# Kernel tuning notes

Measured on AMD Instinct MI355X. Metric: run time of the kernel, lower is better.

Reference implementation:

```python
import jax, jax.numpy as jnp
import numpy as np

N, E, IN, H0, H1 = 50000, 1600000, 64, 64, 128


def _gcn(h, W, b, row, col):
    # PyG GCNConv, add_self_loops=False, unit edge weights:
    # out[col] += d^{-1/2}[row] * d^{-1/2}[col] * (h @ W)[row]; bias added after aggregation
    n = h.shape[0]
    deg = jnp.zeros((n,), h.dtype).at[col].add(jnp.ones((row.shape[0],), h.dtype))
    dinv = jnp.where(deg > 0, jax.lax.rsqrt(jnp.maximum(deg, 1e-12)), 0.0)
    norm = (dinv[row] * dinv[col])[:, None]  # [E,1]
    m = h @ W  # transform before propagate (small GEMM)
    out = jnp.zeros((n, W.shape[1]), h.dtype).at[col].add(norm * m[row])
    return out + b


def _bn(h, g, b):
    # BatchNorm1d training-mode math (biased variance), eps=1e-5
    mu = h.mean(0)
    var = ((h - mu) ** 2).mean(0)
    return g * (h - mu) * jax.lax.rsqrt(var + 1e-5) + b


def _san(h):
    return jnp.nan_to_num(h, nan=0.0, posinf=100.0, neginf=-100.0)


def _slice(x, ei, W0, b0, W1, b1, res1, g0, be0, g1, be1):
    row, col = ei[0], ei[1]
    # layer 0: conv -> bn -> relu -> (dropout=eval identity) -> residual (Identity, 64==64) -> nan_to_num
    h1 = _san(jax.nn.relu(_bn(_gcn(x, W0, b0, row, col), g0, be0)) + x)
    # layer 1 (last): conv -> bn -> residual (Linear proj 64->128, no bias) -> nan_to_num
    h2 = _san(_bn(_gcn(h1, W1, b1, row, col), g1, be1) + h1 @ res1)
    return h2


def setup_inputs() -> dict:
    k = jax.random.split(jax.random.key(0), 16)
    f = lambda kk, sh, s: jax.random.normal(kk, sh, jnp.float32) * s
    return {
        "x": f(k[0], (N, IN), 1.0),
        "edge_index0": jax.random.randint(k[1], (2, E), 0, N),
        "edge_index1": jax.random.randint(k[2], (2, E), 0, N),
        "w0_s0": f(k[3], (IN, H0), 0.1), "b0_s0": jnp.zeros((H0,), jnp.float32),
        "w1_s0": f(k[4], (H0, H1), 0.1), "b1_s0": jnp.zeros((H1,), jnp.float32),
        "res1_s0": f(k[5], (H0, H1), 0.1),
        "w0_s1": f(k[6], (IN, H0), 0.1), "b0_s1": jnp.zeros((H0,), jnp.float32),
        "w1_s1": f(k[7], (H0, H1), 0.1), "b1_s1": jnp.zeros((H1,), jnp.float32),
        "res1_s1": f(k[8], (H0, H1), 0.1),
        "bn_g0": jnp.ones((H0,), jnp.float32), "bn_b0": jnp.zeros((H0,), jnp.float32),
        "bn_g1": jnp.ones((H1,), jnp.float32), "bn_b1": jnp.zeros((H1,), jnp.float32),
        "fc1_w": f(k[9], (2 * H1, H1), 0.1), "fc1_b": jnp.zeros((H1,), jnp.float32),
        "fc2_w": f(k[10], (H1, 2), 0.1), "fc2_b": jnp.zeros((2,), jnp.float32),
    }


def reference(x, edge_index0, edge_index1,
              w0_s0, b0_s0, w1_s0, b1_s0, res1_s0,
              w0_s1, b0_s1, w1_s1, b1_s1, res1_s1,
              bn_g0, bn_b0, bn_g1, bn_b1,
              fc1_w, fc1_b, fc2_w, fc2_b):
    out0 = _slice(x, edge_index0, w0_s0, b0_s0, w1_s0, b1_s0, res1_s0, bn_g0, bn_b0, bn_g1, bn_b1)
    out1 = _slice(x, edge_index1, w0_s1, b0_s1, w1_s1, b1_s1, res1_s1, bn_g0, bn_b0, bn_g1, bn_b1)
    combined = jnp.concatenate([out0, out1], axis=1)  # [N, 2*H1]
    h = jax.nn.relu(combined @ fc1_w + fc1_b)  # dropout is eval-mode identity
    logits = h @ fc2_w + fc2_b
    return logits, jax.nn.softmax(logits, axis=1)
```

## Files before the change

### kernel.cpp

```cpp
#include <hip/hip_runtime.h>
#include <hip/hip_bf16.h>
#include <math.h>


typedef short v8s __attribute__((ext_vector_type(8)));
typedef float f32x4 __attribute__((ext_vector_type(4)));

#define BSTRIDE 10240

__device__ __forceinline__ float sanf(float v) {
    if (v != v) return 0.f;
    if (isinf(v)) return v > 0.f ? 100.f : -100.f;
    return v;
}

__device__ __forceinline__ unsigned short bf16of(float v) {
    __hip_bfloat16 h = __float2bfloat16(v);
    return *(unsigned short*)&h;
}
__device__ __forceinline__ unsigned pack2(float lo, float hi) {
    return (unsigned)bf16of(lo) | ((unsigned)bf16of(hi) << 16);
}
__device__ __forceinline__ float uflo(unsigned u) { return __uint_as_float(u << 16); }
__device__ __forceinline__ float ufhi(unsigned u) { return __uint_as_float(u & 0xFFFF0000u); }
__device__ __forceinline__ float fofbf16(unsigned short u) {
    return __uint_as_float(((unsigned)u) << 16);
}

__device__ __forceinline__ void packone(const float* __restrict__ src, unsigned* __restrict__ dst,
                                        int L, int Khalf, int F) {
    int c = L / Khalf, kp = L - c * Khalf;
    dst[L] = pack2(src[(2 * kp) * F + c], src[(2 * kp + 1) * F + c]);
}

__global__ __launch_bounds__(256) void prep_kernel(const float* __restrict__ w0_0,
                                                   const float* __restrict__ w0_1,
                                                   const float* __restrict__ w1_0,
                                                   const float* __restrict__ w1_1,
                                                   const float* __restrict__ r_0,
                                                   const float* __restrict__ r_1,
                                                   const float* __restrict__ fc1,
                                                   unsigned* __restrict__ wpk,
                                                   int* __restrict__ bcnt,
                                                   float* __restrict__ sums) {
    int gid = blockIdx.x * 256 + threadIdx.x;
    if (gid < 512) bcnt[gid] = 0;
    if (gid < 8192) sums[gid] = 0.f;
    if (gid < 2048)       packone(w0_0, wpk + 0,     gid - 0,     32, 64);
    else if (gid < 4096)  packone(w0_1, wpk + 2048,  gid - 2048,  32, 64);
    else if (gid < 8192)  packone(w1_0, wpk + 4096,  gid - 4096,  32, 128);
    else if (gid < 12288) packone(w1_1, wpk + 8192,  gid - 8192,  32, 128);
    else if (gid < 16384) packone(r_0,  wpk + 12288, gid - 12288, 32, 128);
    else if (gid < 20480) packone(r_1,  wpk + 16384, gid - 16384, 32, 128);
    else if (gid < 36864) packone(fc1,  wpk + 20480, gid - 20480, 128, 128);
}


__global__ __launch_bounds__(512) void kC_bin(const int* __restrict__ ei0,
                                              const int* __restrict__ ei1,
                                              int* __restrict__ bcnt,
                                              unsigned* __restrict__ binned,
                                              int E, int n) {
    __shared__ int cnt[512];
    __shared__ int base[512];
    int t = threadIdx.x;
    cnt[t] = 0;
    int E2 = 2 * E;
    int e0 = blockIdx.x * 8192;
    unsigned pk[16];
    int bk[16];
    __syncthreads();
#pragma unroll
    for (int j = 0; j < 16; ++j) {
        int ge = e0 + t + j * 512;
        bk[j] = -1;
        if (ge < E2) {
            int slice = ge >= E;
            const int* ei = slice ? ei1 : ei0;
            int e = ge - slice * E;
            int col = ei[E + e], row = ei[e];
            int gcol = slice * n + col;
            bk[j] = gcol >> 8;
            pk[j] = (unsigned)row | (((unsigned)gcol & 255u) << 16);
            atomicAdd(&cnt[bk[j]], 1);
        }
    }
    __syncthreads();
    {
        int c = cnt[t];
        base[t] = c ? atomicAdd(&bcnt[t], c) : 0;
    }
    __syncthreads();
    cnt[t] = 0;
    __syncthreads();
#pragma unroll
    for (int j = 0; j < 16; ++j) {
        if (bk[j] >= 0) {
            int loc = atomicAdd(&cnt[bk[j]], 1);
            int off = base[bk[j]] + loc;
            if (off < BSTRIDE) binned[(size_t)bk[j] * BSTRIDE + off] = pk[j];
        }
    }
}

__global__ __launch_bounds__(512) void kD_build(const unsigned* __restrict__ binned,
                                                const int* __restrict__ bcnt,
                                                int* __restrict__ rowptr,
                                                float* __restrict__ dinv,
                                                unsigned short* __restrict__ csr,
                                                int n2, int NB) {
    __shared__ int pref[512];
    __shared__ int cnt[256];
    __shared__ int scn[256];
    __shared__ int cur[256];
    int b = blockIdx.x, t = threadIdx.x;
    pref[t] = (t < NB) ? bcnt[t] : 0;
    __syncthreads();
    for (int off = 1; off < 512; off <<= 1) {
        int u = (t >= off) ? pref[t - off] : 0;
        __syncthreads();
        pref[t] += u;
        __syncthreads();
    }
    int s = (b > 0) ? pref[b - 1] : 0;
    int e = pref[b];
    int m = e - s;
    const unsigned* seg = binned + (size_t)b * BSTRIDE;
    if (t < 256) cnt[t] = 0;
    __syncthreads();
    for (int i = t; i < m; i += 512) atomicAdd(&cnt[(seg[i] >> 16) & 255], 1);
    __syncthreads();
    int v = (t < 256) ? cnt[t] : 0;
    if (t < 256) scn[t] = v;
    __syncthreads();
    for (int off = 1; off < 256; off <<= 1) {
        int u = (t < 256 && t >= off) ? scn[t - off] : 0;
        __syncthreads();
        if (t < 256) scn[t] += u;
        __syncthreads();
    }
    if (t < 256) {
        int excl = scn[t] - v;
        int gcol = b * 256 + t;
        if (gcol < n2) {
            rowptr[gcol] = s + excl;
            dinv[gcol] = v > 0 ? rsqrtf((float)v) : 0.f;
        }
        cur[t] = excl;
    }
    __syncthreads();
    for (int i = t; i < m; i += 512) {
        unsigned p = seg[i];
        int cl = (p >> 16) & 255;
        int pos = s + atomicAdd(&cur[cl], 1);
        csr[pos] = (unsigned short)(p & 0xFFFFu);
    }
    if (b == 0 && t == 0) rowptr[n2] = pref[NB - 1];
}


__global__ __launch_bounds__(256) void prescale_bf(const float* __restrict__ x,
                                                   const float* __restrict__ dinv,
                                                   unsigned short* __restrict__ xsb,
                                                   int n64, int n) {
    int i8 = (blockIdx.x * 256 + threadIdx.x) * 8;
    if (i8 >= n64) return;
    int row = i8 >> 6;
    float4 v0 = *(const float4*)&x[i8];
    float4 v1 = *(const float4*)&x[i8 + 4];
    float d0 = dinv[row], d1 = dinv[n + row];
    uint4 o0, o1;
    o0.x = pack2(v0.x * d0, v0.y * d0); o0.y = pack2(v0.z * d0, v0.w * d0);
    o0.z = pack2(v1.x * d0, v1.y * d0); o0.w = pack2(v1.z * d0, v1.w * d0);
    o1.x = pack2(v0.x * d1, v0.y * d1); o1.y = pack2(v0.z * d1, v0.w * d1);
    o1.z = pack2(v1.x * d1, v1.y * d1); o1.w = pack2(v1.z * d1, v1.w * d1);
    *(uint4*)&xsb[i8] = o0;
    *(uint4*)&xsb[n64 + i8] = o1;
}

#define LOAD8(U, IDX)                                                       \
    do {                                                                    \
        _Pragma("unroll") for (int j = 0; j < 8; ++j) {                     \
            int r = __shfl((IDX), j, 8);                                    \
            (U)[j] = *(const uint4*)&mb[(size_t)r * 64 + l * 8];            \
        }                                                                   \
    } while (0)
#define ZPAD8(U, BB)                                                        \
    do {                                                                    \
        _Pragma("unroll") for (int j = 0; j < 8; ++j)                       \
            if ((BB) + j >= e) { (U)[j].x = 0; (U)[j].y = 0;                \
                                 (U)[j].z = 0; (U)[j].w = 0; }              \
    } while (0)
#define ACC8(U)                                                             \
    do {                                                                    \
        _Pragma("unroll") for (int j = 0; j < 8; ++j) {                     \
            a0 += uflo((U)[j].x); a1 += ufhi((U)[j].x);                     \
            a2 += uflo((U)[j].y); a3 += ufhi((U)[j].y);                     \
            a4 += uflo((U)[j].z); a5 += ufhi((U)[j].z);                     \
            a6 += uflo((U)[j].w); a7 += ufhi((U)[j].w);                     \
        }                                                                   \
    } while (0)

__global__ __launch_bounds__(256) void gatherbf_kernel(const int* __restrict__ rowptr,
                                                       const unsigned short* __restrict__ csr,
                                                       const unsigned short* __restrict__ xsb,
                                                       const float* __restrict__ dinv,
                                                       unsigned short* __restrict__ outb,
                                                       int n) {
    int blk = blockIdx.x;
    int xcd = blk & 7;
    int slice = (xcd >= 4) ? 1 : 0;
    int rank = (blk >> 3) * 4 + (xcd & 3);
    int nodeLocal = rank * 32 + (threadIdx.x >> 3);
    if (nodeLocal >= n) return;
    int node = slice * n + nodeLocal;
    int l = threadIdx.x & 7;
    const unsigned short* mb = xsb + (size_t)slice * n * 64;
    int s = rowptr[node], e = rowptr[node + 1];
    float a0 = 0.f, a1 = 0.f, a2 = 0.f, a3 = 0.f, a4 = 0.f, a5 = 0.f, a6 = 0.f, a7 = 0.f;
    uint4 uA[8], uB[8];
    int b = s;
    if (b + 8 <= e) {
        int ia = csr[b + l];
        LOAD8(uA, ia);
        int bB = b + 8;
        int ib = (bB + l < e) ? (int)csr[bB + l] : 0;
        while (true) {
            bool hasB = (bB < e);
            if (hasB) {
                LOAD8(uB, ib);
                if (bB + 8 > e) ZPAD8(uB, bB);
            }
            int bA2 = bB + 8;
            if (bA2 < e) ia = (bA2 + l < e) ? (int)csr[bA2 + l] : 0;
            ACC8(uA);
            if (!hasB) break;
            bool hasA2 = (bA2 < e);
            if (hasA2) {
                LOAD8(uA, ia);
                if (bA2 + 8 > e) ZPAD8(uA, bA2);
            }
            int bB2 = bA2 + 8;
            if (bB2 < e) ib = (bB2 + l < e) ? (int)csr[bB2 + l] : 0;
            ACC8(uB);
            if (!hasA2) break;
            bB = bB2;
        }
    } else if (b < e) {
        int ia = (b + l < e) ? (int)csr[b + l] : 0;
        LOAD8(uA, ia);
        ZPAD8(uA, b);
        ACC8(uA);
    }
    float d = dinv[node];
    uint4 o;
    o.x = pack2(a0 * d, a1 * d);
    o.y = pack2(a2 * d, a3 * d);
    o.z = pack2(a4 * d, a5 * d);
    o.w = pack2(a6 * d, a7 * d);
    *(uint4*)&outb[(size_t)node * 64 + l * 8] = o;
}


template <int F>
__global__ __launch_bounds__(256) void mfma_gemmb(const unsigned short* __restrict__ Ab,
                                                  const unsigned* __restrict__ WT0,
                                                  const unsigned* __restrict__ WT1,
                                                  unsigned short* __restrict__ Cb,
                                                  float* __restrict__ sums_base,
                                                  int roff, int n) {
    constexpr int NC = F / 16;
    __shared__ float ls[2 * F];
    __shared__ unsigned short stb[64 * F];
    int BPS = (n + 63) >> 6;
    int slice = blockIdx.x >= BPS;
    int sb = blockIdx.x - slice * BPS;
    const unsigned* WT = slice ? WT1 : WT0;
    int row0 = slice * n + sb * 64;
    int rows = min(64, n - sb * 64);
    for (int i = threadIdx.x; i < 2 * F; i += 256) ls[i] = 0.f;
    int w = threadIdx.x >> 6, lane = threadIdx.x & 63, q = lane >> 4, ln = lane & 15;
    const unsigned* A32 = (const unsigned*)Ab;
    size_t arow = (size_t)(row0 + 16 * w + ln) * 32;
    v8s af0 = *(const v8s*)&A32[arow + q * 4];
    v8s af1 = *(const v8s*)&A32[arow + 16 + q * 4];
    f32x4 acc[NC];
#pragma unroll
    for (int ct = 0; ct < NC; ++ct) acc[ct] = {0.f, 0.f, 0.f, 0.f};
#pragma unroll
    for (int ct = 0; ct < NC; ++ct) {
        v8s b0 = *(const v8s*)&WT[(ct * 16 + ln) * 32 + q * 4];
        v8s b1 = *(const v8s*)&WT[(ct * 16 + ln) * 32 + 16 + q * 4];
        acc[ct] = __builtin_amdgcn_mfma_f32_16x16x32_bf16(af0, b0, acc[ct], 0, 0, 0);
        acc[ct] = __builtin_amdgcn_mfma_f32_16x16x32_bf16(af1, b1, acc[ct], 0, 0, 0);
    }
    __syncthreads();
#pragma unroll
    for (int ct = 0; ct < NC; ++ct) {
        float s1 = 0.f, s2 = 0.f;
        int cc = ct * 16 + ln;
#pragma unroll
        for (int i = 0; i < 4; ++i) {
            int r = 16 * w + q * 4 + i;
            stb[r * F + (cc ^ ((r & 7) << 3))] = bf16of(acc[ct][i]);
            if (r < rows) {
                float v = acc[ct][i];
                s1 += v;
                s2 += v * v;
            }
        }
        s1 += __shfl_xor(s1, 16); s1 += __shfl_xor(s1, 32);
        s2 += __shfl_xor(s2, 16); s2 += __shfl_xor(s2, 32);
        if (q == 0) {
            atomicAdd(&ls[cc], s1);
            atomicAdd(&ls[F + cc], s2);
        }
    }
    __syncthreads();
    {
        constexpr int CPT = F / 4;
        int rr = threadIdx.x >> 2, sg = threadIdx.x & 3;
        if (rr < rows) {
            int swz = (rr & 7) << 3;
            int cb = sg * CPT;
            uint4* dst = (uint4*)(Cb + (size_t)(row0 + rr) * F + cb);
#pragma unroll
            for (int jj = 0; jj < CPT / 8; ++jj)
                dst[jj] = *(const uint4*)&stb[rr * F + ((cb + jj * 8) ^ swz)];
        }
    }
    if (threadIdx.x < F) {
        float* dst = sums_base + (blockIdx.x & 7) * 1024 + roff + slice * 2 * F;
        unsafeAtomicAdd(&dst[threadIdx.x], ls[threadIdx.x]);
        unsafeAtomicAdd(&dst[F + threadIdx.x], ls[F + threadIdx.x]);
    }
}

__global__ __launch_bounds__(256) void mfma_apply1(const unsigned short* __restrict__ h1b,
                                                   const unsigned short* __restrict__ Tb,
                                                   const unsigned* __restrict__ RT0,
                                                   const unsigned* __restrict__ RT1,
                                                   const float* __restrict__ sums_base,
                                                   const float* __restrict__ g,
                                                   const float* __restrict__ be,
                                                   unsigned short* __restrict__ comb, int n) {
    __shared__ float st[64 * 128];
    __shared__ float scl[256];
    int BPS = (n + 63) >> 6;
    int slice = blockIdx.x >= BPS;
    int sb = blockIdx.x - slice * BPS;
    const unsigned* WT = slice ? RT1 : RT0;
    int row0 = slice * n + sb * 64;
    int rows = min(64, n - sb * 64);
    int t = threadIdx.x;
    if (t < 128) {
        float s1 = 0.f, s2 = 0.f;
#pragma unroll
        for (int r = 0; r < 8; ++r) {
            const float* src = sums_base + r * 1024 + slice * 256;
            s1 += src[t];
            s2 += src[128 + t];
        }
        float inv_n = 1.0f / (float)n;
        float mu = s1 * inv_n;
        float var = fmaxf(s2 * inv_n - mu * mu, 0.f);
        float scale = g[t] * rsqrtf(var + 1e-5f);
        scl[t] = scale;
        scl[128 + t] = be[t] - mu * scale;
    }
    int w = t >> 6, lane = t & 63, q = lane >> 4, ln = lane & 15;
    const unsigned* A32 = (const unsigned*)h1b;
    size_t arow = (size_t)(row0 + 16 * w + ln) * 32;
    v8s af0 = *(const v8s*)&A32[arow + q * 4];
    v8s af1 = *(const v8s*)&A32[arow + 16 + q * 4];
    f32x4 acc[8];
#pragma unroll
    for (int ct = 0; ct < 8; ++ct) acc[ct] = {0.f, 0.f, 0.f, 0.f};
#pragma unroll
    for (int ct = 0; ct < 8; ++ct) {
        v8s b0 = *(const v8s*)&WT[(ct * 16 + ln) * 32 + q * 4];
        v8s b1 = *(const v8s*)&WT[(ct * 16 + ln) * 32 + 16 + q * 4];
        acc[ct] = __builtin_amdgcn_mfma_f32_16x16x32_bf16(af0, b0, acc[ct], 0, 0, 0);
        acc[ct] = __builtin_amdgcn_mfma_f32_16x16x32_bf16(af1, b1, acc[ct], 0, 0, 0);
    }
#pragma unroll
    for (int ct = 0; ct < 8; ++ct) {
        int cc = ct * 16 + ln;
#pragma unroll
        for (int i = 0; i < 4; ++i) {
            int r = 16 * w + q * 4 + i;
            st[r * 128 + (cc ^ ((r & 7) << 2))] = acc[ct][i];
        }
    }
    __syncthreads();
    int rr = t >> 2, sg = t & 3;
    if (rr >= rows) return;
    int swz = (rr & 7) << 2;
    int rg = row0 + rr;
    const uint4* tbp = (const uint4*)(Tb + (size_t)rg * 128 + sg * 32);
    const float* scb = scl + sg * 32;
    uint4* outp = (uint4*)(comb + (size_t)(rg - slice * n) * 256 + slice * 128 + sg * 32);
#pragma unroll
    for (int jj = 0; jj < 4; ++jj) {
        uint4 tv = tbp[jj];
        int base = sg * 32 + jj * 8;
        float4 a0 = *(const float4*)&st[rr * 128 + (base ^ swz)];
        float4 a1 = *(const float4*)&st[rr * 128 + ((base + 4) ^ swz)];
        float4 s0 = *(const float4*)&scb[jj * 8];
        float4 s1 = *(const float4*)&scb[jj * 8 + 4];
        float4 h0 = *(const float4*)&scb[128 + jj * 8];
        float4 h1v = *(const float4*)&scb[128 + jj * 8 + 4];
        float o0 = sanf(fmaf(uflo(tv.x), s0.x, h0.x) + a0.x);
        float o1 = sanf(fmaf(ufhi(tv.x), s0.y, h0.y) + a0.y);
        float o2 = sanf(fmaf(uflo(tv.y), s0.z, h0.z) + a0.z);
        float o3 = sanf(fmaf(ufhi(tv.y), s0.w, h0.w) + a0.w);
        float o4 = sanf(fmaf(uflo(tv.z), s1.x, h1v.x) + a1.x);
        float o5 = sanf(fmaf(ufhi(tv.z), s1.y, h1v.y) + a1.y);
        float o6 = sanf(fmaf(uflo(tv.w), s1.z, h1v.z) + a1.z);
        float o7 = sanf(fmaf(ufhi(tv.w), s1.w, h1v.w) + a1.w);
        uint4 ov;
        ov.x = pack2(o0, o1);
        ov.y = pack2(o2, o3);
        ov.z = pack2(o4, o5);
        ov.w = pack2(o6, o7);
        outp[jj] = ov;
    }
}

__global__ __launch_bounds__(256) void mfma_head_fc2(const unsigned short* __restrict__ comb,
                                                     const unsigned* __restrict__ FT,
                                                     const float* __restrict__ bias,
                                                     const float* __restrict__ w2,
                                                     const float* __restrict__ b2,
                                                     float* __restrict__ out, int n) {
    int row0 = blockIdx.x * 64;
    int rows = min(64, n - row0);
    int w = threadIdx.x >> 6, lane = threadIdx.x & 63, q = lane >> 4, ln = lane & 15;
    const unsigned* A32 = (const unsigned*)comb;
    size_t arow = (size_t)(row0 + 16 * w + ln) * 128;
    f32x4 acc[8];
#pragma unroll
    for (int ct = 0; ct < 8; ++ct) acc[ct] = {0.f, 0.f, 0.f, 0.f};
#pragma unroll
    for (int kt = 0; kt < 4; ++kt) {
        v8s af0 = *(const v8s*)&A32[arow + kt * 32 + q * 4];
        v8s af1 = *(const v8s*)&A32[arow + kt * 32 + 16 + q * 4];
#pragma unroll
        for (int ct = 0; ct < 8; ++ct) {
            v8s b0 = *(const v8s*)&FT[(ct * 16 + ln) * 128 + kt * 32 + q * 4];
            v8s b1 = *(const v8s*)&FT[(ct * 16 + ln) * 128 + kt * 32 + 16 + q * 4];
            acc[ct] = __builtin_amdgcn_mfma_f32_16x16x32_bf16(af0, b0, acc[ct], 0, 0, 0);
            acc[ct] = __builtin_amdgcn_mfma_f32_16x16x32_bf16(af1, b1, acc[ct], 0, 0, 0);
        }
    }
    float p0[4] = {0.f, 0.f, 0.f, 0.f}, p1[4] = {0.f, 0.f, 0.f, 0.f};
#pragma unroll
    for (int ct = 0; ct < 8; ++ct) {
        int c = ct * 16 + ln;
        float bi = bias[c];
        float w20 = w2[c * 2], w21 = w2[c * 2 + 1];
#pragma unroll
        for (int i = 0; i < 4; ++i) {
            float h = fmaxf(acc[ct][i] + bi, 0.f);
            p0[i] = fmaf(h, w20, p0[i]);
            p1[i] = fmaf(h, w21, p1[i]);
        }
    }
#pragma unroll
    for (int i = 0; i < 4; ++i) {
#pragma unroll
        for (int msk = 1; msk < 16; msk <<= 1) {
            p0[i] += __shfl_xor(p0[i], msk);
            p1[i] += __shfl_xor(p1[i], msk);
        }
    }
    if (ln == 0) {
        float bb0 = b2[0], bb1 = b2[1];
#pragma unroll
        for (int i = 0; i < 4; ++i) {
            int r = 16 * w + q * 4 + i;
            if (r >= rows) continue;
            int R = row0 + r;
            float l0 = p0[i] + bb0, l1 = p1[i] + bb1;
            float mx = fmaxf(l0, l1);
            float e0 = expf(l0 - mx), e1 = expf(l1 - mx);
            float inv = 1.0f / (e0 + e1);
            out[(size_t)R * 2] = l0;
            out[(size_t)R * 2 + 1] = l1;
            out[(size_t)2 * n + R * 2] = e0 * inv;
            out[(size_t)2 * n + R * 2 + 1] = e1 * inv;
        }
    }
}

__global__ __launch_bounds__(256) void apply0_kernel(const unsigned short* __restrict__ t0b,
                                                     const float* __restrict__ x,
                                                     const float* __restrict__ sums_base,
                                                     const float* __restrict__ g,
                                                     const float* __restrict__ be,
                                                     const float* __restrict__ dinv,
                                                     unsigned short* __restrict__ h1b,
                                                     unsigned short* __restrict__ h1sb,
                                                     int n64, int total, int n) {
    __shared__ float sc[256];
    int t = threadIdx.x;
    if (t < 128) {
        int slice = t >> 6, f = t & 63;
        float s1 = 0.f, s2 = 0.f;
#pragma unroll
        for (int r = 0; r < 8; ++r) {
            const float* src = sums_base + r * 1024 + 512 + slice * 128;
            s1 += src[f];
            s2 += src[64 + f];
        }
        float inv_n = 1.0f / (float)n;
        float mu = s1 * inv_n;
        float var = fmaxf(s2 * inv_n - mu * mu, 0.f);
        float scale = g[f] * rsqrtf(var + 1e-5f);
        sc[slice * 128 + f] = scale;
        sc[slice * 128 + 64 + f] = be[f] - mu * scale;
    }
    __syncthreads();
    int i8 = (blockIdx.x * 256 + t) * 8;
    if (i8 >= total) return;
    int slice = i8 >= n64;
    int f0 = i8 & 63;
    const float* scp = sc + slice * 128;
    uint4 tv = *(const uint4*)&t0b[i8];
    const float* xp = x + (i8 - slice * n64);
    float4 x0 = *(const float4*)xp;
    float4 x1 = *(const float4*)(xp + 4);
    float4 s0 = *(const float4*)&scp[f0];
    float4 s1 = *(const float4*)&scp[f0 + 4];
    float4 g0 = *(const float4*)&scp[64 + f0];
    float4 g1 = *(const float4*)&scp[64 + f0 + 4];
    float d = dinv[i8 >> 6];
    float tvv[8] = {uflo(tv.x), ufhi(tv.x), uflo(tv.y), ufhi(tv.y),
                    uflo(tv.z), ufhi(tv.z), uflo(tv.w), ufhi(tv.w)};
    float sa[8] = {s0.x, s0.y, s0.z, s0.w, s1.x, s1.y, s1.z, s1.w};
    float sh[8] = {g0.x, g0.y, g0.z, g0.w, g1.x, g1.y, g1.z, g1.w};
    float xv[8] = {x0.x, x0.y, x0.z, x0.w, x1.x, x1.y, x1.z, x1.w};
    unsigned po[4], ps[4];
#pragma unroll
    for (int j = 0; j < 4; ++j) {
        float a = sanf(fmaxf(fmaf(tvv[2 * j], sa[2 * j], sh[2 * j]), 0.f) + xv[2 * j]);
        float b = sanf(fmaxf(fmaf(tvv[2 * j + 1], sa[2 * j + 1], sh[2 * j + 1]), 0.f) + xv[2 * j + 1]);
        po[j] = pack2(a, b);
        ps[j] = pack2(a * d, b * d);
    }
    *(uint4*)&h1b[i8] = *(uint4*)po;
    *(uint4*)&h1sb[i8] = *(uint4*)ps;
}

static inline int cdiv(int a, int b) { return (a + b - 1) / b; }

extern "C" void kernel_launch(void* const* d_in, const int* in_sizes, int n_in,
                              void* d_out, int out_size, void* d_ws, size_t ws_size,
                              hipStream_t stream) {
    const float* x       = (const float*)d_in[0];
    const int*   ei0     = (const int*)d_in[1];
    const int*   ei1     = (const int*)d_in[2];
    const float* w0_s0   = (const float*)d_in[3];
    const float* w1_s0   = (const float*)d_in[5];
    const float* res1_s0 = (const float*)d_in[7];
    const float* w0_s1   = (const float*)d_in[8];
    const float* w1_s1   = (const float*)d_in[10];
    const float* res1_s1 = (const float*)d_in[12];
    const float* bn_g0   = (const float*)d_in[13];
    const float* bn_b0   = (const float*)d_in[14];
    const float* bn_g1   = (const float*)d_in[15];
    const float* bn_b1   = (const float*)d_in[16];
    const float* fc1_w   = (const float*)d_in[17];
    const float* fc1_b   = (const float*)d_in[18];
    const float* fc2_w   = (const float*)d_in[19];
    const float* fc2_b   = (const float*)d_in[20];
    float* out = (float*)d_out;

    int n = in_sizes[0] / 64;
    int E = in_sizes[1] / 2;
    int n2 = 2 * n, E2 = 2 * E;
    int n64 = n * 64;
    int NB = cdiv(n2, 256);
    int BPS = cdiv(n, 64);
    int GB = 8 * cdiv(cdiv(n, 32), 4);

    float* X1 = (float*)d_ws;
    float* S  = X1 + (size_t)n2 * 64;
    unsigned short* Gb   = (unsigned short*)(S + (size_t)n2 * 64);
    unsigned short* h1b  = Gb + (size_t)n2 * 64;
    unsigned short* comb = h1b + (size_t)n2 * 64;
    unsigned short* xsb  = comb + (size_t)n * 256;
    float* dinv = (float*)(xsb + (size_t)n * 128);
    float* sums = dinv + n2;
    float* scsh = sums + 8192;
    unsigned* wpk = (unsigned*)(scsh + 512);
    unsigned short* csr = (unsigned short*)(wpk + 36864);
    int* rowptr = (int*)(csr + (size_t)E2);
    int* bcnt   = rowptr + (n2 + 1);
    unsigned short* t0b = (unsigned short*)X1;
    unsigned short* Tb  = (unsigned short*)X1;
    unsigned* binned = (unsigned*)comb;
    unsigned short* h1sb = (unsigned short*)S;
    unsigned* w0T0 = wpk + 0,    *w0T1 = wpk + 2048;
    unsigned* w1T0 = wpk + 4096, *w1T1 = wpk + 8192;
    unsigned* rT0  = wpk + 12288,*rT1  = wpk + 16384;
    unsigned* fT   = wpk + 20480;

    prep_kernel<<<144, 256, 0, stream>>>(w0_s0, w0_s1, w1_s0, w1_s1,
                                         res1_s0, res1_s1, fc1_w, wpk, bcnt, sums);
    kC_bin<<<cdiv(E2, 8192), 512, 0, stream>>>(ei0, ei1, bcnt, binned, E, n);
    kD_build<<<NB, 512, 0, stream>>>(binned, bcnt, rowptr, dinv, csr, n2, NB);

    prescale_bf<<<cdiv(n64, 2048), 256, 0, stream>>>(x, dinv, xsb, n64, n);
    gatherbf_kernel<<<GB, 256, 0, stream>>>(rowptr, csr, xsb, dinv, Gb, n);
    mfma_gemmb<64><<<2 * BPS, 256, 0, stream>>>(Gb, w0T0, w0T1, t0b, sums, 512, n);
    apply0_kernel<<<cdiv(2 * n64, 2048), 256, 0, stream>>>(t0b, x, sums, bn_g0, bn_b0,
                                                           dinv, h1b, h1sb, n64, 2 * n64, n);

    gatherbf_kernel<<<GB, 256, 0, stream>>>(rowptr, csr, h1sb, dinv, Gb, n);
    mfma_gemmb<128><<<2 * BPS, 256, 0, stream>>>(Gb, w1T0, w1T1, Tb, sums, 0, n);
    mfma_apply1<<<2 * BPS, 256, 0, stream>>>(h1b, Tb, rT0, rT1, sums, bn_g1, bn_b1, comb, n);

    mfma_head_fc2<<<BPS, 256, 0, stream>>>(comb, fT, fc1_b, fc2_w, fc2_b, out, n);
}
```

Before: 353.5 us.

## Fuse all stages into one persistent cooperative kernel with grid syncs

Replaces the chain of ten separate kernel launches (prep, binning, CSR build, prescale, two gathers, two GEMMs, the two apply steps and the head) with a single persistent cooperative kernel. The stages are separated by grid-wide barriers and run as grid-stride loops over tiles, with shared memory reused through a union. The aim is to remove launch overhead and inter-kernel gaps. In exchange, grid size is capped by occupancy, barriers become grid syncs, per-block work changes (for example the binning chunk size), and register pressure from the merged kernel may lower occupancy.

```diff
diff --git a/kernel.cpp b/kernel.cpp
--- a/kernel.cpp
+++ b/kernel.cpp
@@ -1,6 +1,9 @@
 #include <hip/hip_runtime.h>
 #include <hip/hip_bf16.h>
+#include <hip/hip_cooperative_groups.h>
 #include <math.h>
+
+namespace cg = cooperative_groups;
 
 
 typedef short v8s __attribute__((ext_vector_type(8)));
@@ -13,7 +16,6 @@
     if (isinf(v)) return v > 0.f ? 100.f : -100.f;
     return v;
 }
-
 __device__ __forceinline__ unsigned short bf16of(float v) {
     __hip_bfloat16 h = __float2bfloat16(v);
     return *(unsigned short*)&h;
@@ -23,159 +25,35 @@
 }
 __device__ __forceinline__ float uflo(unsigned u) { return __uint_as_float(u << 16); }
 __device__ __forceinline__ float ufhi(unsigned u) { return __uint_as_float(u & 0xFFFF0000u); }
-__device__ __forceinline__ float fofbf16(unsigned short u) {
-    return __uint_as_float(((unsigned)u) << 16);
-}
+
+struct Params {
+    const float* x;
+    const int *ei0, *ei1;
+    const float *w0_0, *w0_1, *w1_0, *w1_1, *r_0, *r_1, *fc1;
+    const float *bn_g0, *bn_b0, *bn_g1, *bn_b1;
+    const float *fc1_b, *fc2_w, *fc2_b;
+    float* out;
+    unsigned short* t0b;
+    unsigned short *Gb, *h1b, *comb, *xsb, *h1sb;
+    float *dinv, *sums;
+    unsigned* wpk;
+    unsigned short* csr;
+    int *rowptr, *bcnt;
+    unsigned* binned;
+    int n, E, NB, BPS;
+};
+
+union SMemU {
+    struct { int cnt[512]; int base[512]; } c;
+    struct { int red[256]; int cnt[256]; int scn[256]; int cur[256]; } d;
+    struct { unsigned short stb[64 * 128]; } g;
+    struct { float st[64 * 128]; } a1;
+};
 
 __device__ __forceinline__ void packone(const float* __restrict__ src, unsigned* __restrict__ dst,
                                         int L, int Khalf, int F) {
     int c = L / Khalf, kp = L - c * Khalf;
     dst[L] = pack2(src[(2 * kp) * F + c], src[(2 * kp + 1) * F + c]);
-}
-
-__global__ __launch_bounds__(256) void prep_kernel(const float* __restrict__ w0_0,
-                                                   const float* __restrict__ w0_1,
-                                                   const float* __restrict__ w1_0,
-                                                   const float* __restrict__ w1_1,
-                                                   const float* __restrict__ r_0,
-                                                   const float* __restrict__ r_1,
-                                                   const float* __restrict__ fc1,
-                                                   unsigned* __restrict__ wpk,
-                                                   int* __restrict__ bcnt,
-                                                   float* __restrict__ sums) {
-    int gid = blockIdx.x * 256 + threadIdx.x;
-    if (gid < 512) bcnt[gid] = 0;
-    if (gid < 8192) sums[gid] = 0.f;
-    if (gid < 2048)       packone(w0_0, wpk + 0,     gid - 0,     32, 64);
-    else if (gid < 4096)  packone(w0_1, wpk + 2048,  gid - 2048,  32, 64);
-    else if (gid < 8192)  packone(w1_0, wpk + 4096,  gid - 4096,  32, 128);
-    else if (gid < 12288) packone(w1_1, wpk + 8192,  gid - 8192,  32, 128);
-    else if (gid < 16384) packone(r_0,  wpk + 12288, gid - 12288, 32, 128);
-    else if (gid < 20480) packone(r_1,  wpk + 16384, gid - 16384, 32, 128);
-    else if (gid < 36864) packone(fc1,  wpk + 20480, gid - 20480, 128, 128);
-}
-
-
-__global__ __launch_bounds__(512) void kC_bin(const int* __restrict__ ei0,
-                                              const int* __restrict__ ei1,
-                                              int* __restrict__ bcnt,
-                                              unsigned* __restrict__ binned,
-                                              int E, int n) {
-    __shared__ int cnt[512];
-    __shared__ int base[512];
-    int t = threadIdx.x;
-    cnt[t] = 0;
-    int E2 = 2 * E;
-    int e0 = blockIdx.x * 8192;
-    unsigned pk[16];
-    int bk[16];
-    __syncthreads();
-#pragma unroll
-    for (int j = 0; j < 16; ++j) {
-        int ge = e0 + t + j * 512;
-        bk[j] = -1;
-        if (ge < E2) {
-            int slice = ge >= E;
-            const int* ei = slice ? ei1 : ei0;
-            int e = ge - slice * E;
-            int col = ei[E + e], row = ei[e];
-            int gcol = slice * n + col;
-            bk[j] = gcol >> 8;
-            pk[j] = (unsigned)row | (((unsigned)gcol & 255u) << 16);
-            atomicAdd(&cnt[bk[j]], 1);
-        }
-    }
-    __syncthreads();
-    {
-        int c = cnt[t];
-        base[t] = c ? atomicAdd(&bcnt[t], c) : 0;
-    }
-    __syncthreads();
-    cnt[t] = 0;
-    __syncthreads();
-#pragma unroll
-    for (int j = 0; j < 16; ++j) {
-        if (bk[j] >= 0) {
-            int loc = atomicAdd(&cnt[bk[j]], 1);
-            int off = base[bk[j]] + loc;
-            if (off < BSTRIDE) binned[(size_t)bk[j] * BSTRIDE + off] = pk[j];
-        }
-    }
-}
-
-__global__ __launch_bounds__(512) void kD_build(const unsigned* __restrict__ binned,
-                                                const int* __restrict__ bcnt,
-                                                int* __restrict__ rowptr,
-                                                float* __restrict__ dinv,
-                                                unsigned short* __restrict__ csr,
-                                                int n2, int NB) {
-    __shared__ int pref[512];
-    __shared__ int cnt[256];
-    __shared__ int scn[256];
-    __shared__ int cur[256];
-    int b = blockIdx.x, t = threadIdx.x;
-    pref[t] = (t < NB) ? bcnt[t] : 0;
-    __syncthreads();
-    for (int off = 1; off < 512; off <<= 1) {
-        int u = (t >= off) ? pref[t - off] : 0;
-        __syncthreads();
-        pref[t] += u;
-        __syncthreads();
-    }
-    int s = (b > 0) ? pref[b - 1] : 0;
-    int e = pref[b];
-    int m = e - s;
-    const unsigned* seg = binned + (size_t)b * BSTRIDE;
-    if (t < 256) cnt[t] = 0;
-    __syncthreads();
-    for (int i = t; i < m; i += 512) atomicAdd(&cnt[(seg[i] >> 16) & 255], 1);
-    __syncthreads();
-    int v = (t < 256) ? cnt[t] : 0;
-    if (t < 256) scn[t] = v;
-    __syncthreads();
-    for (int off = 1; off < 256; off <<= 1) {
-        int u = (t < 256 && t >= off) ? scn[t - off] : 0;
-        __syncthreads();
-        if (t < 256) scn[t] += u;
-        __syncthreads();
-    }
-    if (t < 256) {
-        int excl = scn[t] - v;
-        int gcol = b * 256 + t;
-        if (gcol < n2) {
-            rowptr[gcol] = s + excl;
-            dinv[gcol] = v > 0 ? rsqrtf((float)v) : 0.f;
-        }
-        cur[t] = excl;
-    }
-    __syncthreads();
-    for (int i = t; i < m; i += 512) {
-        unsigned p = seg[i];
-        int cl = (p >> 16) & 255;
-        int pos = s + atomicAdd(&cur[cl], 1);
-        csr[pos] = (unsigned short)(p & 0xFFFFu);
-    }
-    if (b == 0 && t == 0) rowptr[n2] = pref[NB - 1];
-}
-
-
-__global__ __launch_bounds__(256) void prescale_bf(const float* __restrict__ x,
-                                                   const float* __restrict__ dinv,
-                                                   unsigned short* __restrict__ xsb,
-                                                   int n64, int n) {
-    int i8 = (blockIdx.x * 256 + threadIdx.x) * 8;
-    if (i8 >= n64) return;
-    int row = i8 >> 6;
-    float4 v0 = *(const float4*)&x[i8];
-    float4 v1 = *(const float4*)&x[i8 + 4];
-    float d0 = dinv[row], d1 = dinv[n + row];
-    uint4 o0, o1;
-    o0.x = pack2(v0.x * d0, v0.y * d0); o0.y = pack2(v0.z * d0, v0.w * d0);
-    o0.z = pack2(v1.x * d0, v1.y * d0); o0.w = pack2(v1.z * d0, v1.w * d0);
-    o1.x = pack2(v0.x * d1, v0.y * d1); o1.y = pack2(v0.z * d1, v0.w * d1);
-    o1.z = pack2(v1.x * d1, v1.y * d1); o1.w = pack2(v1.z * d1, v1.w * d1);
-    *(uint4*)&xsb[i8] = o0;
-    *(uint4*)&xsb[n64 + i8] = o1;
 }
 
 #define LOAD8(U, IDX)                                                       \
@@ -201,21 +79,12 @@
         }                                                                   \
     } while (0)
 
-__global__ __launch_bounds__(256) void gatherbf_kernel(const int* __restrict__ rowptr,
-                                                       const unsigned short* __restrict__ csr,
-                                                       const unsigned short* __restrict__ xsb,
-                                                       const float* __restrict__ dinv,
-                                                       unsigned short* __restrict__ outb,
-                                                       int n) {
-    int blk = blockIdx.x;
-    int xcd = blk & 7;
-    int slice = (xcd >= 4) ? 1 : 0;
-    int rank = (blk >> 3) * 4 + (xcd & 3);
-    int nodeLocal = rank * 32 + (threadIdx.x >> 3);
-    if (nodeLocal >= n) return;
-    int node = slice * n + nodeLocal;
-    int l = threadIdx.x & 7;
-    const unsigned short* mb = xsb + (size_t)slice * n * 64;
+__device__ __forceinline__ void gather_node(const int* __restrict__ rowptr,
+                                            const unsigned short* __restrict__ csr,
+                                            const unsigned short* __restrict__ mb,
+                                            const float* __restrict__ dinv,
+                                            int node, int l,
+                                            unsigned short* __restrict__ outrow) {
     int s = rowptr[node], e = rowptr[node + 1];
     float a0 = 0.f, a1 = 0.f, a2 = 0.f, a3 = 0.f, a4 = 0.f, a5 = 0.f, a6 = 0.f, a7 = 0.f;
     uint4 uA[8], uB[8];
@@ -258,298 +127,444 @@
     o.y = pack2(a2 * d, a3 * d);
     o.z = pack2(a4 * d, a5 * d);
     o.w = pack2(a6 * d, a7 * d);
-    *(uint4*)&outb[(size_t)node * 64 + l * 8] = o;
-}
-
+    *(uint4*)&outrow[l * 8] = o;
+}
 
 template <int F>
-__global__ __launch_bounds__(256) void mfma_gemmb(const unsigned short* __restrict__ Ab,
-                                                  const unsigned* __restrict__ WT0,
-                                                  const unsigned* __restrict__ WT1,
-                                                  unsigned short* __restrict__ Cb,
-                                                  float* __restrict__ sums_base,
-                                                  int roff, int n) {
+__device__ __forceinline__ void gemm_tiles(const unsigned short* __restrict__ Ab,
+                                           const unsigned* __restrict__ WT0,
+                                           const unsigned* __restrict__ WT1,
+                                           unsigned short* __restrict__ Cb,
+                                           float* __restrict__ sums,
+                                           int roff, int n, int BPS,
+                                           unsigned short* stb, float* ls) {
     constexpr int NC = F / 16;
-    __shared__ float ls[2 * F];
-    __shared__ unsigned short stb[64 * F];
-    int BPS = (n + 63) >> 6;
-    int slice = blockIdx.x >= BPS;
-    int sb = blockIdx.x - slice * BPS;
-    const unsigned* WT = slice ? WT1 : WT0;
-    int row0 = slice * n + sb * 64;
-    int rows = min(64, n - sb * 64);
-    for (int i = threadIdx.x; i < 2 * F; i += 256) ls[i] = 0.f;
-    int w = threadIdx.x >> 6, lane = threadIdx.x & 63, q = lane >> 4, ln = lane & 15;
-    const unsigned* A32 = (const unsigned*)Ab;
-    size_t arow = (size_t)(row0 + 16 * w + ln) * 32;
-    v8s af0 = *(const v8s*)&A32[arow + q * 4];
-    v8s af1 = *(const v8s*)&A32[arow + 16 + q * 4];
-    f32x4 acc[NC];
-#pragma unroll
-    for (int ct = 0; ct < NC; ++ct) acc[ct] = {0.f, 0.f, 0.f, 0.f};
-#pragma unroll
-    for (int ct = 0; ct < NC; ++ct) {
-        v8s b0 = *(const v8s*)&WT[(ct * 16 + ln) * 32 + q * 4];
-        v8s b1 = *(const v8s*)&WT[(ct * 16 + ln) * 32 + 16 + q * 4];
-        acc[ct] = __builtin_amdgcn_mfma_f32_16x16x32_bf16(af0, b0, acc[ct], 0, 0, 0);
-        acc[ct] = __builtin_amdgcn_mfma_f32_16x16x32_bf16(af1, b1, acc[ct], 0, 0, 0);
-    }
-    __syncthreads();
-#pragma unroll
-    for (int ct = 0; ct < NC; ++ct) {
+    const int t = threadIdx.x;
+    const int G = gridDim.x;
+    for (int tile = blockIdx.x; tile < 2 * BPS; tile += G) {
+        int slice = tile >= BPS;
+        int sb = tile - slice * BPS;
+        const unsigned* WT = slice ? WT1 : WT0;
+        int row0 = slice * n + sb * 64;
+        int rows = min(64, n - sb * 64);
+        for (int i = t; i < 2 * F; i += 256) ls[i] = 0.f;
+        int w = t >> 6, lane = t & 63, q = lane >> 4, ln = lane & 15;
+        const unsigned* A32 = (const unsigned*)Ab;
+        size_t arow = (size_t)(row0 + 16 * w + ln) * 32;
+        v8s af0 = *(const v8s*)&A32[arow + q * 4];
+        v8s af1 = *(const v8s*)&A32[arow + 16 + q * 4];
+        f32x4 acc[NC];
+#pragma unroll
+        for (int ct = 0; ct < NC; ++ct) acc[ct] = {0.f, 0.f, 0.f, 0.f};
+#pragma unroll
+        for (int ct = 0; ct < NC; ++ct) {
+            v8s b0 = *(const v8s*)&WT[(ct * 16 + ln) * 32 + q * 4];
+            v8s b1 = *(const v8s*)&WT[(ct * 16 + ln) * 32 + 16 + q * 4];
+            acc[ct] = __builtin_amdgcn_mfma_f32_16x16x32_bf16(af0, b0, acc[ct], 0, 0, 0);
+            acc[ct] = __builtin_amdgcn_mfma_f32_16x16x32_bf16(af1, b1, acc[ct], 0, 0, 0);
+        }
+        __syncthreads();
+#pragma unroll
+        for (int ct = 0; ct < NC; ++ct) {
+            float s1 = 0.f, s2 = 0.f;
+            int cc = ct * 16 + ln;
+#pragma unroll
+            for (int i = 0; i < 4; ++i) {
+                int r = 16 * w + q * 4 + i;
+                stb[r * F + (cc ^ ((r & 7) << 3))] = bf16of(acc[ct][i]);
+                if (r < rows) {
+                    float v = acc[ct][i];
+                    s1 += v;
+                    s2 += v * v;
+                }
+            }
+            s1 += __shfl_xor(s1, 16); s1 += __shfl_xor(s1, 32);
+            s2 += __shfl_xor(s2, 16); s2 += __shfl_xor(s2, 32);
+            if (q == 0) {
+                atomicAdd(&ls[cc], s1);
+                atomicAdd(&ls[F + cc], s2);
+            }
+        }
+        __syncthreads();
+        {
+            constexpr int CPT = F / 4;
+            int rr = t >> 2, sg = t & 3;
+            if (rr < rows) {
+                int swz = (rr & 7) << 3;
+                int cb = sg * CPT;
+                uint4* dst = (uint4*)(Cb + (size_t)(row0 + rr) * F + cb);
+#pragma unroll
+                for (int jj = 0; jj < CPT / 8; ++jj)
+                    dst[jj] = *(const uint4*)&stb[rr * F + ((cb + jj * 8) ^ swz)];
+            }
+        }
+        if (t < F) {
+            float* dst = sums + (blockIdx.x & 7) * 1024 + roff + slice * 2 * F;
+            unsafeAtomicAdd(&dst[t], ls[t]);
+            unsafeAtomicAdd(&dst[F + t], ls[F + t]);
+        }
+        __syncthreads();
+    }
+}
+
+__global__ __launch_bounds__(256, 4) void fused_all(Params p) {
+    cg::grid_group grid = cg::this_grid();
+    __shared__ SMemU sm;
+    __shared__ float scl[512];
+    const int t = threadIdx.x;
+    const int bid = blockIdx.x;
+    const int G = gridDim.x;
+    const int n = p.n, E = p.E;
+    const int n2 = 2 * n, E2 = 2 * E, n64 = n * 64;
+    const int NB = p.NB, BPS = p.BPS;
+    unsigned* w0T0 = p.wpk + 0,    *w0T1 = p.wpk + 2048;
+    unsigned* w1T0 = p.wpk + 4096, *w1T1 = p.wpk + 8192;
+    unsigned* rT0  = p.wpk + 12288,*rT1  = p.wpk + 16384;
+    unsigned* fT   = p.wpk + 20480;
+
+    for (int gid = bid * 256 + t; gid < 36864; gid += G * 256) {
+        if (gid < 512) p.bcnt[gid] = 0;
+        if (gid < 8192) p.sums[gid] = 0.f;
+        if (gid < 2048)       packone(p.w0_0, p.wpk + 0,     gid - 0,     32, 64);
+        else if (gid < 4096)  packone(p.w0_1, p.wpk + 2048,  gid - 2048,  32, 64);
+        else if (gid < 8192)  packone(p.w1_0, p.wpk + 4096,  gid - 4096,  32, 128);
+        else if (gid < 12288) packone(p.w1_1, p.wpk + 8192,  gid - 8192,  32, 128);
+        else if (gid < 16384) packone(p.r_0,  p.wpk + 12288, gid - 12288, 32, 128);
+        else if (gid < 20480) packone(p.r_1,  p.wpk + 16384, gid - 16384, 32, 128);
+        else                  packone(p.fc1,  p.wpk + 20480, gid - 20480, 128, 128);
+    }
+    grid.sync();
+
+    {
+        int nch = (E2 + 4095) >> 12;
+        for (int ch = bid; ch < nch; ch += G) {
+            sm.c.cnt[t] = 0; sm.c.cnt[t + 256] = 0;
+            __syncthreads();
+            unsigned pk[16]; int bk[16];
+            int e0 = ch * 4096;
+#pragma unroll
+            for (int j = 0; j < 16; ++j) {
+                int ge = e0 + t + j * 256;
+                bk[j] = -1;
+                if (ge < E2) {
+                    int slice = ge >= E;
+                    const int* ei = slice ? p.ei1 : p.ei0;
+                    int e = ge - slice * E;
+                    int col = ei[E + e], row = ei[e];
+                    int gcol = slice * n + col;
+                    bk[j] = gcol >> 8;
+                    pk[j] = (unsigned)row | (((unsigned)gcol & 255u) << 16);
+                    atomicAdd(&sm.c.cnt[bk[j]], 1);
+                }
+            }
+            __syncthreads();
+            for (int i = t; i < 512; i += 256) {
+                int c = sm.c.cnt[i];
+                sm.c.base[i] = c ? atomicAdd(&p.bcnt[i], c) : 0;
+            }
+            __syncthreads();
+            sm.c.cnt[t] = 0; sm.c.cnt[t + 256] = 0;
+            __syncthreads();
+#pragma unroll
+            for (int j = 0; j < 16; ++j) {
+                if (bk[j] >= 0) {
+                    int loc = atomicAdd(&sm.c.cnt[bk[j]], 1);
+                    int off = sm.c.base[bk[j]] + loc;
+                    if (off < BSTRIDE) p.binned[(size_t)bk[j] * BSTRIDE + off] = pk[j];
+                }
+            }
+            __syncthreads();
+        }
+    }
+    grid.sync();
+
+    for (int b = bid; b < NB; b += G) {
+        int partial = 0;
+        for (int i = t; i < b; i += 256) partial += p.bcnt[i];
+        sm.d.red[t] = partial;
+        __syncthreads();
+        for (int off = 128; off > 0; off >>= 1) {
+            if (t < off) sm.d.red[t] += sm.d.red[t + off];
+            __syncthreads();
+        }
+        int s = sm.d.red[0];
+        int e = s + p.bcnt[b];
+        int m = e - s;
+        const unsigned* seg = p.binned + (size_t)b * BSTRIDE;
+        sm.d.cnt[t] = 0;
+        __syncthreads();
+        for (int i = t; i < m; i += 256) atomicAdd(&sm.d.cnt[(seg[i] >> 16) & 255], 1);
+        __syncthreads();
+        int v = sm.d.cnt[t];
+        sm.d.scn[t] = v;
+        __syncthreads();
+        for (int off = 1; off < 256; off <<= 1) {
+            int u = (t >= off) ? sm.d.scn[t - off] : 0;
+            __syncthreads();
+            sm.d.scn[t] += u;
+            __syncthreads();
+        }
+        {
+            int excl = sm.d.scn[t] - v;
+            int gcol = b * 256 + t;
+            if (gcol < n2) {
+                p.rowptr[gcol] = s + excl;
+                p.dinv[gcol] = v > 0 ? rsqrtf((float)v) : 0.f;
+            }
+            sm.d.cur[t] = excl;
+        }
+        __syncthreads();
+        for (int i = t; i < m; i += 256) {
+            unsigned pkv = seg[i];
+            int cl = (pkv >> 16) & 255;
+            int pos = s + atomicAdd(&sm.d.cur[cl], 1);
+            p.csr[pos] = (unsigned short)(pkv & 0xFFFFu);
+        }
+        if (b == NB - 1 && t == 0) p.rowptr[n2] = e;
+        __syncthreads();
+    }
+    grid.sync();
+
+    for (int i8 = (bid * 256 + t) * 8; i8 < n64; i8 += G * 256 * 8) {
+        int row = i8 >> 6;
+        float4 v0 = *(const float4*)&p.x[i8];
+        float4 v1 = *(const float4*)&p.x[i8 + 4];
+        float d0 = p.dinv[row], d1 = p.dinv[n + row];
+        uint4 o0, o1;
+        o0.x = pack2(v0.x * d0, v0.y * d0); o0.y = pack2(v0.z * d0, v0.w * d0);
+        o0.z = pack2(v1.x * d0, v1.y * d0); o0.w = pack2(v1.z * d0, v1.w * d0);
+        o1.x = pack2(v0.x * d1, v0.y * d1); o1.y = pack2(v0.z * d1, v0.w * d1);
+        o1.z = pack2(v1.x * d1, v1.y * d1); o1.w = pack2(v1.z * d1, v1.w * d1);
+        *(uint4*)&p.xsb[i8] = o0;
+        *(uint4*)&p.xsb[n64 + i8] = o1;
+    }
+    grid.sync();
+
+    {
+        int l = t & 7;
+        for (int base = bid * 32; base < n2; base += G * 32) {
+            int node = base + (t >> 3);
+            if (node < n2) {
+                const unsigned short* mb = p.xsb + (size_t)((node >= n) ? n : 0) * 64;
+                gather_node(p.rowptr, p.csr, mb, p.dinv, node, l, p.Gb + (size_t)node * 64);
+            }
+        }
+    }
+    grid.sync();
+
+    gemm_tiles<64>(p.Gb, w0T0, w0T1, p.t0b, p.sums, 512, n, BPS, sm.g.stb, scl);
+    grid.sync();
+
+    if (t < 128) {
+        int slice = t >> 6, f = t & 63;
         float s1 = 0.f, s2 = 0.f;
-        int cc = ct * 16 + ln;
-#pragma unroll
-        for (int i = 0; i < 4; ++i) {
-            int r = 16 * w + q * 4 + i;
-            stb[r * F + (cc ^ ((r & 7) << 3))] = bf16of(acc[ct][i]);
-            if (r < rows) {
-                float v = acc[ct][i];
-                s1 += v;
-                s2 += v * v;
-            }
-        }
-        s1 += __shfl_xor(s1, 16); s1 += __shfl_xor(s1, 32);
-        s2 += __shfl_xor(s2, 16); s2 += __shfl_xor(s2, 32);
-        if (q == 0) {
-            atomicAdd(&ls[cc], s1);
-            atomicAdd(&ls[F + cc], s2);
-        }
-    }
-    __syncthreads();
-    {
-        constexpr int CPT = F / 4;
-        int rr = threadIdx.x >> 2, sg = threadIdx.x & 3;
-        if (rr < rows) {
-            int swz = (rr & 7) << 3;
-            int cb = sg * CPT;
-            uint4* dst = (uint4*)(Cb + (size_t)(row0 + rr) * F + cb);
-#pragma unroll
-            for (int jj = 0; jj < CPT / 8; ++jj)
-                dst[jj] = *(const uint4*)&stb[rr * F + ((cb + jj * 8) ^ swz)];
-        }
-    }
-    if (threadIdx.x < F) {
-        float* dst = sums_base + (blockIdx.x & 7) * 1024 + roff + slice * 2 * F;
-        unsafeAtomicAdd(&dst[threadIdx.x], ls[threadIdx.x]);
-        unsafeAtomicAdd(&dst[F + threadIdx.x], ls[F + threadIdx.x]);
-    }
-}
-
-__global__ __launch_bounds__(256) void mfma_apply1(const unsigned short* __restrict__ h1b,
-                                                   const unsigned short* __restrict__ Tb,
-                                                   const unsigned* __restrict__ RT0,
-                                                   const unsigned* __restrict__ RT1,
-                                                   const float* __restrict__ sums_base,
-                                                   const float* __restrict__ g,
-                                                   const float* __restrict__ be,
-                                                   unsigned short* __restrict__ comb, int n) {
-    __shared__ float st[64 * 128];
-    __shared__ float scl[256];
-    int BPS = (n + 63) >> 6;
-    int slice = blockIdx.x >= BPS;
-    int sb = blockIdx.x - slice * BPS;
-    const unsigned* WT = slice ? RT1 : RT0;
-    int row0 = slice * n + sb * 64;
-    int rows = min(64, n - sb * 64);
-    int t = threadIdx.x;
-    if (t < 128) {
-        float s1 = 0.f, s2 = 0.f;
 #pragma unroll
         for (int r = 0; r < 8; ++r) {
-            const float* src = sums_base + r * 1024 + slice * 256;
-            s1 += src[t];
-            s2 += src[128 + t];
+            const float* src = p.sums + r * 1024 + 512 + slice * 128;
+            s1 += src[f];
+            s2 += src[64 + f];
         }
         float inv_n = 1.0f / (float)n;
         float mu = s1 * inv_n;
         float var = fmaxf(s2 * inv_n - mu * mu, 0.f);
-        float scale = g[t] * rsqrtf(var + 1e-5f);
-        scl[t] = scale;
-        scl[128 + t] = be[t] - mu * scale;
-    }
-    int w = t >> 6, lane = t & 63, q = lane >> 4, ln = lane & 15;
-    const unsigned* A32 = (const unsigned*)h1b;
-    size_t arow = (size_t)(row0 + 16 * w + ln) * 32;
-    v8s af0 = *(const v8s*)&A32[arow + q * 4];
-    v8s af1 = *(const v8s*)&A32[arow + 16 + q * 4];
-    f32x4 acc[8];
-#pragma unroll
-    for (int ct = 0; ct < 8; ++ct) acc[ct] = {0.f, 0.f, 0.f, 0.f};
-#pragma unroll
-    for (int ct = 0; ct < 8; ++ct) {
-        v8s b0 = *(const v8s*)&WT[(ct * 16 + ln) * 32 + q * 4];
-        v8s b1 = *(const v8s*)&WT[(ct * 16 + ln) * 32 + 16 + q * 4];
-        acc[ct] = __builtin_amdgcn_mfma_f32_16x16x32_bf16(af0, b0, acc[ct], 0, 0, 0);
-        acc[ct] = __builtin_amdgcn_mfma_f32_16x16x32_bf16(af1, b1, acc[ct], 0, 0, 0);
-    }
-#pragma unroll
-    for (int ct = 0; ct < 8; ++ct) {
-        int cc = ct * 16 + ln;
-#pragma unroll
-        for (int i = 0; i < 4; ++i) {
-            int r = 16 * w + q * 4 + i;
-            st[r * 128 + (cc ^ ((r & 7) << 2))] = acc[ct][i];
-        }
+        float scale = p.bn_g0[f] * rsqrtf(var + 1e-5f);
+        scl[slice * 128 + f] = scale;
+        scl[slice * 128 + 64 + f] = p.bn_b0[f] - mu * scale;
     }
     __syncthreads();
-    int rr = t >> 2, sg = t & 3;
-    if (rr >= rows) return;
-    int swz = (rr & 7) << 2;
-    int rg = row0 + rr;
-    const uint4* tbp = (const uint4*)(Tb + (size_t)rg * 128 + sg * 32);
-    const float* scb = scl + sg * 32;
-    uint4* outp = (uint4*)(comb + (size_t)(rg - slice * n) * 256 + slice * 128 + sg * 32);
-#pragma unroll
-    for (int jj = 0; jj < 4; ++jj) {
-        uint4 tv = tbp[jj];
-        int base = sg * 32 + jj * 8;
-        float4 a0 = *(const float4*)&st[rr * 128 + (base ^ swz)];
-        float4 a1 = *(const float4*)&st[rr * 128 + ((base + 4) ^ swz)];
-        float4 s0 = *(const float4*)&scb[jj * 8];
-        float4 s1 = *(const float4*)&scb[jj * 8 + 4];
-        float4 h0 = *(const float4*)&scb[128 + jj * 8];
-        float4 h1v = *(const float4*)&scb[128 + jj * 8 + 4];
-        float o0 = sanf(fmaf(uflo(tv.x), s0.x, h0.x) + a0.x);
-        float o1 = sanf(fmaf(ufhi(tv.x), s0.y, h0.y) + a0.y);
-        float o2 = sanf(fmaf(uflo(tv.y), s0.z, h0.z) + a0.z);
-        float o3 = sanf(fmaf(ufhi(tv.y), s0.w, h0.w) + a0.w);
-        float o4 = sanf(fmaf(uflo(tv.z), s1.x, h1v.x) + a1.x);
-        float o5 = sanf(fmaf(ufhi(tv.z), s1.y, h1v.y) + a1.y);
-        float o6 = sanf(fmaf(uflo(tv.w), s1.z, h1v.z) + a1.z);
-        float o7 = sanf(fmaf(ufhi(tv.w), s1.w, h1v.w) + a1.w);
-        uint4 ov;
-        ov.x = pack2(o0, o1);
-        ov.y = pack2(o2, o3);
-        ov.z = pack2(o4, o5);
-        ov.w = pack2(o6, o7);
-        outp[jj] = ov;
-    }
-}
-
-__global__ __launch_bounds__(256) void mfma_head_fc2(const unsigned short* __restrict__ comb,
-                                                     const unsigned* __restrict__ FT,
-                                                     const float* __restrict__ bias,
-                                                     const float* __restrict__ w2,
-                                                     const float* __restrict__ b2,
-                                                     float* __restrict__ out, int n) {
-    int row0 = blockIdx.x * 64;
-    int rows = min(64, n - row0);
-    int w = threadIdx.x >> 6, lane = threadIdx.x & 63, q = lane >> 4, ln = lane & 15;
-    const unsigned* A32 = (const unsigned*)comb;
-    size_t arow = (size_t)(row0 + 16 * w + ln) * 128;
-    f32x4 acc[8];
-#pragma unroll
-    for (int ct = 0; ct < 8; ++ct) acc[ct] = {0.f, 0.f, 0.f, 0.f};
-#pragma unroll
-    for (int kt = 0; kt < 4; ++kt) {
-        v8s af0 = *(const v8s*)&A32[arow + kt * 32 + q * 4];
-        v8s af1 = *(const v8s*)&A32[arow + kt * 32 + 16 + q * 4];
-#pragma unroll
-        for (int ct = 0; ct < 8; ++ct) {
-            v8s b0 = *(const v8s*)&FT[(ct * 16 + ln) * 128 + kt * 32 + q * 4];
-            v8s b1 = *(const v8s*)&FT[(ct * 16 + ln) * 128 + kt * 32 + 16 + q * 4];
-            acc[ct] = __builtin_amdgcn_mfma_f32_16x16x32_bf16(af0, b0, acc[ct], 0, 0, 0);
-            acc[ct] = __builtin_amdgcn_mfma_f32_16x16x32_bf16(af1, b1, acc[ct], 0, 0, 0);
-        }
-    }
-    float p0[4] = {0.f, 0.f, 0.f, 0.f}, p1[4] = {0.f, 0.f, 0.f, 0.f};
-#pragma unroll
-    for (int ct = 0; ct < 8; ++ct) {
-        int c = ct * 16 + ln;
-        float bi = bias[c];
-        float w20 = w2[c * 2], w21 = w2[c * 2 + 1];
-#pragma unroll
-        for (int i = 0; i < 4; ++i) {
-            float h = fmaxf(acc[ct][i] + bi, 0.f);
-            p0[i] = fmaf(h, w20, p0[i]);
-            p1[i] = fmaf(h, w21, p1[i]);
-        }
-    }
-#pragma unroll
-    for (int i = 0; i < 4; ++i) {
-#pragma unroll
-        for (int msk = 1; msk < 16; msk <<= 1) {
-            p0[i] += __shfl_xor(p0[i], msk);
-            p1[i] += __shfl_xor(p1[i], msk);
-        }
-    }
-    if (ln == 0) {
-        float bb0 = b2[0], bb1 = b2[1];
-#pragma unroll
-        for (int i = 0; i < 4; ++i) {
-            int r = 16 * w + q * 4 + i;
-            if (r >= rows) continue;
-            int R = row0 + r;
-            float l0 = p0[i] + bb0, l1 = p1[i] + bb1;
-            float mx = fmaxf(l0, l1);
-            float e0 = expf(l0 - mx), e1 = expf(l1 - mx);
-            float inv = 1.0f / (e0 + e1);
-            out[(size_t)R * 2] = l0;
-            out[(size_t)R * 2 + 1] = l1;
-            out[(size_t)2 * n + R * 2] = e0 * inv;
-            out[(size_t)2 * n + R * 2 + 1] = e1 * inv;
-        }
-    }
-}
-
-__global__ __launch_bounds__(256) void apply0_kernel(const unsigned short* __restrict__ t0b,
-                                                     const float* __restrict__ x,
-                                                     const float* __restrict__ sums_base,
-                                                     const float* __restrict__ g,
-                                                     const float* __restrict__ be,
-                                                     const float* __restrict__ dinv,
-                                                     unsigned short* __restrict__ h1b,
-                                                     unsigned short* __restrict__ h1sb,
-                                                     int n64, int total, int n) {
-    __shared__ float sc[256];
-    int t = threadIdx.x;
-    if (t < 128) {
-        int slice = t >> 6, f = t & 63;
+    for (int i8 = (bid * 256 + t) * 8; i8 < 2 * n64; i8 += G * 256 * 8) {
+        int slice = i8 >= n64;
+        int f0 = i8 & 63;
+        const float* scp = scl + slice * 128;
+        uint4 tv = *(const uint4*)&p.t0b[i8];
+        const float* xp = p.x + (i8 - slice * n64);
+        float4 x0 = *(const float4*)xp;
+        float4 x1 = *(const float4*)(xp + 4);
+        float4 s0 = *(const float4*)&scp[f0];
+        float4 s1 = *(const float4*)&scp[f0 + 4];
+        float4 g0 = *(const float4*)&scp[64 + f0];
+        float4 g1 = *(const float4*)&scp[64 + f0 + 4];
+        float d = p.dinv[i8 >> 6];
+        float tvv[8] = {uflo(tv.x), ufhi(tv.x), uflo(tv.y), ufhi(tv.y),
+                        uflo(tv.z), ufhi(tv.z), uflo(tv.w), ufhi(tv.w)};
+        float sa[8] = {s0.x, s0.y, s0.z, s0.w, s1.x, s1.y, s1.z, s1.w};
+        float sh[8] = {g0.x, g0.y, g0.z, g0.w, g1.x, g1.y, g1.z, g1.w};
+        float xv[8] = {x0.x, x0.y, x0.z, x0.w, x1.x, x1.y, x1.z, x1.w};
+        unsigned po[4], ps[4];
+#pragma unroll
+        for (int j = 0; j < 4; ++j) {
+            float a = sanf(fmaxf(fmaf(tvv[2 * j], sa[2 * j], sh[2 * j]), 0.f) + xv[2 * j]);
+            float b2 = sanf(fmaxf(fmaf(tvv[2 * j + 1], sa[2 * j + 1], sh[2 * j + 1]), 0.f) + xv[2 * j + 1]);
+            po[j] = pack2(a, b2);
+            ps[j] = pack2(a * d, b2 * d);
+        }
+        *(uint4*)&p.h1b[i8] = *(uint4*)po;
+        *(uint4*)&p.h1sb[i8] = *(uint4*)ps;
+    }
+    grid.sync();
+
+    {
+        int l = t & 7;
+        for (int base = bid * 32; base < n2; base += G * 32) {
+            int node = base + (t >> 3);
+            if (node < n2) {
+                const unsigned short* mb = p.h1sb + (size_t)((node >= n) ? n : 0) * 64;
+                gather_node(p.rowptr, p.csr, mb, p.dinv, node, l, p.Gb + (size_t)node * 64);
+            }
+        }
+    }
+    grid.sync();
+
+    gemm_tiles<128>(p.Gb, w1T0, w1T1, p.t0b , p.sums, 0, n, BPS, sm.g.stb, scl);
+    grid.sync();
+
+    {
+        int slice = t >> 7, f = t & 127;
         float s1 = 0.f, s2 = 0.f;
 #pragma unroll
         for (int r = 0; r < 8; ++r) {
-            const float* src = sums_base + r * 1024 + 512 + slice * 128;
+            const float* src = p.sums + r * 1024 + slice * 256;
             s1 += src[f];
-            s2 += src[64 + f];
+            s2 += src[128 + f];
         }
         float inv_n = 1.0f / (float)n;
         float mu = s1 * inv_n;
         float var = fmaxf(s2 * inv_n - mu * mu, 0.f);
+        const float* g = p.bn_g1;
+        const float* be = p.bn_b1;
         float scale = g[f] * rsqrtf(var + 1e-5f);
-        sc[slice * 128 + f] = scale;
-        sc[slice * 128 + 64 + f] = be[f] - mu * scale;
+        scl[slice * 256 + f] = scale;
+        scl[slice * 256 + 128 + f] = be[f] - mu * scale;
     }
     __syncthreads();
-    int i8 = (blockIdx.x * 256 + t) * 8;
-    if (i8 >= total) return;
-    int slice = i8 >= n64;
-    int f0 = i8 & 63;
-    const float* scp = sc + slice * 128;
-    uint4 tv = *(const uint4*)&t0b[i8];
-    const float* xp = x + (i8 - slice * n64);
-    float4 x0 = *(const float4*)xp;
-    float4 x1 = *(const float4*)(xp + 4);
-    float4 s0 = *(const float4*)&scp[f0];
-    float4 s1 = *(const float4*)&scp[f0 + 4];
-    float4 g0 = *(const float4*)&scp[64 + f0];
-    float4 g1 = *(const float4*)&scp[64 + f0 + 4];
-    float d = dinv[i8 >> 6];
-    float tvv[8] = {uflo(tv.x), ufhi(tv.x), uflo(tv.y), ufhi(tv.y),
-                    uflo(tv.z), ufhi(tv.z), uflo(tv.w), ufhi(tv.w)};
-    float sa[8] = {s0.x, s0.y, s0.z, s0.w, s1.x, s1.y, s1.z, s1.w};
-    float sh[8] = {g0.x, g0.y, g0.z, g0.w, g1.x, g1.y, g1.z, g1.w};
-    float xv[8] = {x0.x, x0.y, x0.z, x0.w, x1.x, x1.y, x1.z, x1.w};
-    unsigned po[4], ps[4];
-#pragma unroll
-    for (int j = 0; j < 4; ++j) {
-        float a = sanf(fmaxf(fmaf(tvv[2 * j], sa[2 * j], sh[2 * j]), 0.f) + xv[2 * j]);
-        float b = sanf(fmaxf(fmaf(tvv[2 * j + 1], sa[2 * j + 1], sh[2 * j + 1]), 0.f) + xv[2 * j + 1]);
-        po[j] = pack2(a, b);
-        ps[j] = pack2(a * d, b * d);
-    }
-    *(uint4*)&h1b[i8] = *(uint4*)po;
-    *(uint4*)&h1sb[i8] = *(uint4*)ps;
+    for (int tile = bid; tile < 2 * BPS; tile += G) {
+        int slice = tile >= BPS;
+        int sb = tile - slice * BPS;
+        const unsigned* WT = slice ? rT1 : rT0;
+        int row0 = slice * n + sb * 64;
+        int rows = min(64, n - sb * 64);
+        int w = t >> 6, lane = t & 63, q = lane >> 4, ln = lane & 15;
+        const unsigned* A32 = (const unsigned*)p.h1b;
+        size_t arow = (size_t)(row0 + 16 * w + ln) * 32;
+        v8s af0 = *(const v8s*)&A32[arow + q * 4];
+        v8s af1 = *(const v8s*)&A32[arow + 16 + q * 4];
+        f32x4 acc[8];
+#pragma unroll
+        for (int ct = 0; ct < 8; ++ct) acc[ct] = {0.f, 0.f, 0.f, 0.f};
+#pragma unroll
+        for (int ct = 0; ct < 8; ++ct) {
+            v8s b0 = *(const v8s*)&WT[(ct * 16 + ln) * 32 + q * 4];
+            v8s b1 = *(const v8s*)&WT[(ct * 16 + ln) * 32 + 16 + q * 4];
+            acc[ct] = __builtin_amdgcn_mfma_f32_16x16x32_bf16(af0, b0, acc[ct], 0, 0, 0);
+            acc[ct] = __builtin_amdgcn_mfma_f32_16x16x32_bf16(af1, b1, acc[ct], 0, 0, 0);
+        }
+#pragma unroll
+        for (int ct = 0; ct < 8; ++ct) {
+            int cc = ct * 16 + ln;
+#pragma unroll
+            for (int i = 0; i < 4; ++i) {
+                int r = 16 * w + q * 4 + i;
+                sm.a1.st[r * 128 + (cc ^ ((r & 7) << 2))] = acc[ct][i];
+            }
+        }
+        __syncthreads();
+        int rr = t >> 2, sg = t & 3;
+        if (rr < rows) {
+            int swz = (rr & 7) << 2;
+            int rg = row0 + rr;
+            const uint4* tbp = (const uint4*)(p.t0b + (size_t)rg * 128 + sg * 32);
+            const float* scb = scl + slice * 256 + sg * 32;
+            uint4* outp = (uint4*)(p.comb + (size_t)(rg - slice * n) * 256 + slice * 128 + sg * 32);
+#pragma unroll
+            for (int jj = 0; jj < 4; ++jj) {
+                uint4 tv = tbp[jj];
+                int base = sg * 32 + jj * 8;
+                float4 a0 = *(const float4*)&sm.a1.st[rr * 128 + (base ^ swz)];
+                float4 a1 = *(const float4*)&sm.a1.st[rr * 128 + ((base + 4) ^ swz)];
+                float4 s0 = *(const float4*)&scb[jj * 8];
+                float4 s1 = *(const float4*)&scb[jj * 8 + 4];
+                float4 h0 = *(const float4*)&scb[128 + jj * 8];
+                float4 h1v = *(const float4*)&scb[128 + jj * 8 + 4];
+                float o0 = sanf(fmaf(uflo(tv.x), s0.x, h0.x) + a0.x);
+                float o1 = sanf(fmaf(ufhi(tv.x), s0.y, h0.y) + a0.y);
+                float o2 = sanf(fmaf(uflo(tv.y), s0.z, h0.z) + a0.z);
+                float o3 = sanf(fmaf(ufhi(tv.y), s0.w, h0.w) + a0.w);
+                float o4 = sanf(fmaf(uflo(tv.z), s1.x, h1v.x) + a1.x);
+                float o5 = sanf(fmaf(ufhi(tv.z), s1.y, h1v.y) + a1.y);
+                float o6 = sanf(fmaf(uflo(tv.w), s1.z, h1v.z) + a1.z);
+                float o7 = sanf(fmaf(ufhi(tv.w), s1.w, h1v.w) + a1.w);
+                uint4 ov;
+                ov.x = pack2(o0, o1);
+                ov.y = pack2(o2, o3);
+                ov.z = pack2(o4, o5);
+                ov.w = pack2(o6, o7);
+                outp[jj] = ov;
+            }
+        }
+        __syncthreads();
+    }
+    grid.sync();
+
+    for (int tile = bid; tile < BPS; tile += G) {
+        int row0 = tile * 64;
+        int rows = min(64, n - row0);
+        int w = t >> 6, lane = t & 63, q = lane >> 4, ln = lane & 15;
+        const unsigned* A32 = (const unsigned*)p.comb;
+        size_t arow = (size_t)(row0 + 16 * w + ln) * 128;
+        f32x4 acc[8];
+#pragma unroll
+        for (int ct = 0; ct < 8; ++ct) acc[ct] = {0.f, 0.f, 0.f, 0.f};
+#pragma unroll
+        for (int kt = 0; kt < 4; ++kt) {
+            v8s af0 = *(const v8s*)&A32[arow + kt * 32 + q * 4];
+            v8s af1 = *(const v8s*)&A32[arow + kt * 32 + 16 + q * 4];
+#pragma unroll
+            for (int ct = 0; ct < 8; ++ct) {
+                v8s b0 = *(const v8s*)&fT[(ct * 16 + ln) * 128 + kt * 32 + q * 4];
+                v8s b1 = *(const v8s*)&fT[(ct * 16 + ln) * 128 + kt * 32 + 16 + q * 4];
+                acc[ct] = __builtin_amdgcn_mfma_f32_16x16x32_bf16(af0, b0, acc[ct], 0, 0, 0);
+                acc[ct] = __builtin_amdgcn_mfma_f32_16x16x32_bf16(af1, b1, acc[ct], 0, 0, 0);
+            }
+        }
+        float p0[4] = {0.f, 0.f, 0.f, 0.f}, p1[4] = {0.f, 0.f, 0.f, 0.f};
+#pragma unroll
+        for (int ct = 0; ct < 8; ++ct) {
+            int c = ct * 16 + ln;
+            float bi = p.fc1_b[c];
+            float w20 = p.fc2_w[c * 2], w21 = p.fc2_w[c * 2 + 1];
+#pragma unroll
+            for (int i = 0; i < 4; ++i) {
+                float h = fmaxf(acc[ct][i] + bi, 0.f);
+                p0[i] = fmaf(h, w20, p0[i]);
+                p1[i] = fmaf(h, w21, p1[i]);
+            }
+        }
+#pragma unroll
+        for (int i = 0; i < 4; ++i) {
+#pragma unroll
+            for (int msk = 1; msk < 16; msk <<= 1) {
+                p0[i] += __shfl_xor(p0[i], msk);
+                p1[i] += __shfl_xor(p1[i], msk);
+            }
+        }
+        if (ln == 0) {
+            float bb0 = p.fc2_b[0], bb1 = p.fc2_b[1];
+#pragma unroll
+            for (int i = 0; i < 4; ++i) {
+                int r = 16 * w + q * 4 + i;
+                if (r >= rows) continue;
+                int R = row0 + r;
+                float l0 = p0[i] + bb0, l1 = p1[i] + bb1;
+                float mx = fmaxf(l0, l1);
+                float e0 = expf(l0 - mx), e1 = expf(l1 - mx);
+                float inv = 1.0f / (e0 + e1);
+                p.out[(size_t)R * 2] = l0;
+                p.out[(size_t)R * 2 + 1] = l1;
+                p.out[(size_t)2 * n + R * 2] = e0 * inv;
+                p.out[(size_t)2 * n + R * 2 + 1] = e1 * inv;
+            }
+        }
+    }
 }
 
 static inline int cdiv(int a, int b) { return (a + b - 1) / b; }
@@ -557,32 +572,32 @@
 extern "C" void kernel_launch(void* const* d_in, const int* in_sizes, int n_in,
                               void* d_out, int out_size, void* d_ws, size_t ws_size,
                               hipStream_t stream) {
-    const float* x       = (const float*)d_in[0];
-    const int*   ei0     = (const int*)d_in[1];
-    const int*   ei1     = (const int*)d_in[2];
-    const float* w0_s0   = (const float*)d_in[3];
-    const float* w1_s0   = (const float*)d_in[5];
-    const float* res1_s0 = (const float*)d_in[7];
-    const float* w0_s1   = (const float*)d_in[8];
-    const float* w1_s1   = (const float*)d_in[10];
-    const float* res1_s1 = (const float*)d_in[12];
-    const float* bn_g0   = (const float*)d_in[13];
-    const float* bn_b0   = (const float*)d_in[14];
-    const float* bn_g1   = (const float*)d_in[15];
-    const float* bn_b1   = (const float*)d_in[16];
-    const float* fc1_w   = (const float*)d_in[17];
-    const float* fc1_b   = (const float*)d_in[18];
-    const float* fc2_w   = (const float*)d_in[19];
-    const float* fc2_b   = (const float*)d_in[20];
-    float* out = (float*)d_out;
+    Params hp;
+    hp.x     = (const float*)d_in[0];
+    hp.ei0   = (const int*)d_in[1];
+    hp.ei1   = (const int*)d_in[2];
+    hp.w0_0  = (const float*)d_in[3];
+    hp.w1_0  = (const float*)d_in[5];
+    hp.r_0   = (const float*)d_in[7];
+    hp.w0_1  = (const float*)d_in[8];
+    hp.w1_1  = (const float*)d_in[10];
+    hp.r_1   = (const float*)d_in[12];
+    hp.bn_g0 = (const float*)d_in[13];
+    hp.bn_b0 = (const float*)d_in[14];
+    hp.bn_g1 = (const float*)d_in[15];
+    hp.bn_b1 = (const float*)d_in[16];
+    hp.fc1   = (const float*)d_in[17];
+    hp.fc1_b = (const float*)d_in[18];
+    hp.fc2_w = (const float*)d_in[19];
+    hp.fc2_b = (const float*)d_in[20];
+    hp.out   = (float*)d_out;
 
     int n = in_sizes[0] / 64;
     int E = in_sizes[1] / 2;
     int n2 = 2 * n, E2 = 2 * E;
-    int n64 = n * 64;
-    int NB = cdiv(n2, 256);
-    int BPS = cdiv(n, 64);
-    int GB = 8 * cdiv(cdiv(n, 32), 4);
+    hp.n = n; hp.E = E;
+    hp.NB = cdiv(n2, 256);
+    hp.BPS = cdiv(n, 64);
 
     float* X1 = (float*)d_ws;
     float* S  = X1 + (size_t)n2 * 64;
@@ -597,29 +612,31 @@
     unsigned short* csr = (unsigned short*)(wpk + 36864);
     int* rowptr = (int*)(csr + (size_t)E2);
     int* bcnt   = rowptr + (n2 + 1);
-    unsigned short* t0b = (unsigned short*)X1;
-    unsigned short* Tb  = (unsigned short*)X1;
-    unsigned* binned = (unsigned*)comb;
-    unsigned short* h1sb = (unsigned short*)S;
-    unsigned* w0T0 = wpk + 0,    *w0T1 = wpk + 2048;
-    unsigned* w1T0 = wpk + 4096, *w1T1 = wpk + 8192;
-    unsigned* rT0  = wpk + 12288,*rT1  = wpk + 16384;
-    unsigned* fT   = wpk + 20480;
-
-    prep_kernel<<<144, 256, 0, stream>>>(w0_s0, w0_s1, w1_s0, w1_s1,
-                                         res1_s0, res1_s1, fc1_w, wpk, bcnt, sums);
-    kC_bin<<<cdiv(E2, 8192), 512, 0, stream>>>(ei0, ei1, bcnt, binned, E, n);
-    kD_build<<<NB, 512, 0, stream>>>(binned, bcnt, rowptr, dinv, csr, n2, NB);
-
-    prescale_bf<<<cdiv(n64, 2048), 256, 0, stream>>>(x, dinv, xsb, n64, n);
-    gatherbf_kernel<<<GB, 256, 0, stream>>>(rowptr, csr, xsb, dinv, Gb, n);
-    mfma_gemmb<64><<<2 * BPS, 256, 0, stream>>>(Gb, w0T0, w0T1, t0b, sums, 512, n);
-    apply0_kernel<<<cdiv(2 * n64, 2048), 256, 0, stream>>>(t0b, x, sums, bn_g0, bn_b0,
-                                                           dinv, h1b, h1sb, n64, 2 * n64, n);
-
-    gatherbf_kernel<<<GB, 256, 0, stream>>>(rowptr, csr, h1sb, dinv, Gb, n);
-    mfma_gemmb<128><<<2 * BPS, 256, 0, stream>>>(Gb, w1T0, w1T1, Tb, sums, 0, n);
-    mfma_apply1<<<2 * BPS, 256, 0, stream>>>(h1b, Tb, rT0, rT1, sums, bn_g1, bn_b1, comb, n);
-
-    mfma_head_fc2<<<BPS, 256, 0, stream>>>(comb, fT, fc1_b, fc2_w, fc2_b, out, n);
-}
+
+    hp.t0b = (unsigned short*)X1;
+    hp.Gb = Gb; hp.h1b = h1b; hp.comb = comb; hp.xsb = xsb;
+    hp.h1sb = (unsigned short*)S;
+    hp.dinv = dinv; hp.sums = sums; hp.wpk = wpk;
+    hp.csr = csr; hp.rowptr = rowptr; hp.bcnt = bcnt;
+    hp.binned = (unsigned*)comb;
+
+    static int grid = 0;
+    if (grid == 0) {
+        int maxB = 0;
+        hipError_t err = hipOccupancyMaxActiveBlocksPerMultiprocessor(
+            &maxB, reinterpret_cast<const void*>(&fused_all), 256, 0);
+        if (err != hipSuccess || maxB < 1) maxB = 2;
+        int cu = 256;
+        hipDeviceProp_t prop;
+        int dev = 0;
+        if (hipGetDevice(&dev) == hipSuccess &&
+            hipGetDeviceProperties(&prop, dev) == hipSuccess)
+            cu = prop.multiProcessorCount;
+        grid = maxB * cu;
+        if (grid > 2048) grid = 2048;
+    }
+
+    void* args[] = {(void*)&hp};
+    hipLaunchCooperativeKernel(reinterpret_cast<const void*>(&fused_all),
+                               dim3(grid), dim3(256), args, 0, stream);
+}
```

After: 1.103 ms. 212% more time.
